# Kernel tuning notes

Measured on AMD Instinct MI355X. Metric: run time of the kernel, lower is better.

## Reference

```python
import jax, jax.numpy as jnp
import numpy as np

B, N, M = 4, 8192, 8192


def setup_inputs() -> dict:
    key = jax.random.key(0)
    k1, k2 = jax.random.split(key)
    xyz1 = jax.random.normal(k1, (B, N, 3), dtype=jnp.float32)
    xyz2 = jax.random.normal(k2, (B, M, 3), dtype=jnp.float32)
    return {"xyz1": xyz1, "xyz2": xyz2}


def reference(xyz1, xyz2):
    # Note: torch.cdist(p=2) returns sqrt(sq); min over sqrt == min over sq
    # (monotone), and the module squares afterward, so min of squared
    # distances is exactly equivalent (and avoids sqrt-at-0 grad issues).
    sq1 = jnp.sum(xyz1 * xyz1, axis=-1)  # (B, N)
    sq2 = jnp.sum(xyz2 * xyz2, axis=-1)  # (B, M)
    cross = jnp.einsum("bnd,bmd->bnm", xyz1, xyz2)  # (B, N, M)
    d2 = jnp.maximum(sq1[:, :, None] + sq2[:, None, :] - 2.0 * cross, 0.0)
    dist1 = jnp.min(d2, axis=2)  # (B, N) nearest in xyz2 for each xyz1 point
    dist2 = jnp.min(d2, axis=1)  # (B, M) nearest in xyz1 for each xyz2 point
    return jnp.mean(dist1) + jnp.mean(dist2)
```

## Files before the change

kernel.cpp:

```cpp
#include <hip/hip_runtime.h>
#include <math.h>

typedef short  bf16x8 __attribute__((ext_vector_type(8)));
typedef float  f32x16 __attribute__((ext_vector_type(16)));

constexpr int BATCH = 4, NPTS = 8192;
constexpr int CLOUD = BATCH * NPTS;

__device__ inline unsigned short bf16_rne(float x) {
    unsigned int u = __float_as_uint(x);
    return (unsigned short)((u + 0x7FFFu + ((u >> 16) & 1u)) >> 16);
}
__device__ inline float bf16_val(unsigned short h) {
    return __uint_as_float(((unsigned int)h) << 16);
}

__global__ __launch_bounds__(256) void cd_prep(
    const float* __restrict__ x1, const float* __restrict__ x2,
    uint4* __restrict__ APK, uint4* __restrict__ BPK,
    unsigned int* __restrict__ dist) {
    const int i = blockIdx.x * 256 + threadIdx.x;
    dist[i] = 0x7F800000u;
    const float* src = (i < CLOUD) ? x1 : x2;
    const int idx = i & (CLOUD - 1);
    const float x = src[idx*3+0], y = src[idx*3+1], z = src[idx*3+2];
    const float r = x*x + y*y + z*z;

    const unsigned short one = 0x3F80u;
    const unsigned short r0 = bf16_rne(r);
    const float rm1 = r - bf16_val(r0);
    const unsigned short r1 = bf16_rne(rm1);
    const unsigned short r2 = bf16_rne(rm1 - bf16_val(r1));

    const unsigned short hx = bf16_rne(x), hy = bf16_rne(y), hz = bf16_rne(z);
    const unsigned short lx = bf16_rne(x - bf16_val(hx));
    const unsigned short ly = bf16_rne(y - bf16_val(hy));
    const unsigned short lz = bf16_rne(z - bf16_val(hz));
    uint4 a0, a1;
    a0.x = (unsigned)hx | ((unsigned)lx << 16);
    a0.y = (unsigned)hx | ((unsigned)hy << 16);
    a0.z = (unsigned)ly | ((unsigned)hy << 16);
    a0.w = (unsigned)hz | ((unsigned)lz << 16);
    a1.x = (unsigned)hz | ((unsigned)one << 16);
    a1.y = (unsigned)one | ((unsigned)one << 16);
    a1.z = (unsigned)r0 | ((unsigned)r1 << 16);
    a1.w = (unsigned)r2;

    const float tx = -2.f*x, ty = -2.f*y, tz = -2.f*z;
    const unsigned short ax = bf16_rne(tx), ay = bf16_rne(ty), az = bf16_rne(tz);
    const unsigned short bx = bf16_rne(tx - bf16_val(ax));
    const unsigned short by = bf16_rne(ty - bf16_val(ay));
    const unsigned short bz = bf16_rne(tz - bf16_val(az));
    uint4 b0, b1;
    b0.x = (unsigned)ax | ((unsigned)ax << 16);
    b0.y = (unsigned)bx | ((unsigned)ay << 16);
    b0.z = (unsigned)ay | ((unsigned)by << 16);
    b0.w = (unsigned)az | ((unsigned)az << 16);
    b1.x = (unsigned)bz | ((unsigned)r0 << 16);
    b1.y = (unsigned)r1 | ((unsigned)r2 << 16);
    b1.z = (unsigned)one | ((unsigned)one << 16);
    b1.w = (unsigned)one;

    const int g = i >> 5, w = i & 31;
    APK[g*64 + w]      = a0;  APK[g*64 + 32 + w] = a1;
    BPK[g*64 + w]      = b0;  BPK[g*64 + 32 + w] = b1;
}

__global__ __launch_bounds__(256) void cd_gemm(
    const uint4* __restrict__ APK, const uint4* __restrict__ BPK,
    unsigned int* __restrict__ dist) {

    __shared__ uint4 Blds[2048];
    __shared__ float lbuf[4][32][33];

    const int tid = threadIdx.x;
    const int wv  = tid >> 6;
    const int l   = tid & 63;
    const int lane31 = l & 31, half = l >> 5;

    const int wid = blockIdx.x * 4 + wv;
    const int dir = wid >> 12;
    const int b   = (wid >> 10) & 3;
    const int cc  = (wid >> 7) & 7;
    const int rg  = wid & 127;

    const int aPt = (dir ? CLOUD : 0) + b * NPTS + rg * 64;
    const int bPt = (dir ? 0 : CLOUD) + b * NPTS + cc * 1024;

    {
        const uint4* src = BPK + (size_t)bPt * 2;
#pragma unroll
        for (int k = 0; k < 8; ++k)
            Blds[tid + k * 256] = src[tid + k * 256];
    }

    bf16x8 afr0, afr1;
    {
        uint4 v0 = APK[(size_t)aPt * 2 + l];
        uint4 v1 = APK[(size_t)aPt * 2 + 64 + l];
        __builtin_memcpy(&afr0, &v0, 16);
        __builtin_memcpy(&afr1, &v1, 16);
    }

    f32x16 zc;
#pragma unroll
    for (int i = 0; i < 16; ++i) zc[i] = 0.0f;

    float racc[2][16];
#pragma unroll
    for (int f = 0; f < 2; ++f)
#pragma unroll
        for (int r = 0; r < 16; ++r) racc[f][r] = INFINITY;

    __syncthreads();

#pragma unroll 4
    for (int p = 0; p < 16; ++p) {
        bf16x8 ba, bb;
        uint4 ua = Blds[(2*p + 0) * 64 + l];
        uint4 ub = Blds[(2*p + 1) * 64 + l];
        __builtin_memcpy(&ba, &ua, 16);
        __builtin_memcpy(&bb, &ub, 16);
        f32x16 c0 = __builtin_amdgcn_mfma_f32_32x32x16_bf16(afr0, ba, zc, 0, 0, 0);
        f32x16 c1 = __builtin_amdgcn_mfma_f32_32x32x16_bf16(afr0, bb, zc, 0, 0, 0);
        f32x16 c2 = __builtin_amdgcn_mfma_f32_32x32x16_bf16(afr1, ba, zc, 0, 0, 0);
        f32x16 c3 = __builtin_amdgcn_mfma_f32_32x32x16_bf16(afr1, bb, zc, 0, 0, 0);
#pragma unroll
        for (int r = 0; r < 16; ++r) {
            racc[0][r] = fminf(fminf(c0[r], c1[r]), racc[0][r]);
            racc[1][r] = fminf(fminf(c2[r], c3[r]), racc[1][r]);
        }
    }

    const int distBase = dir * CLOUD + b * NPTS + rg * 64;
#pragma unroll
    for (int f = 0; f < 2; ++f) {
#pragma unroll
        for (int r = 0; r < 16; ++r) {
            const int rl = (r & 3) + 8 * (r >> 2) + 4 * half;
            lbuf[wv][rl][lane31] = racc[f][r];
        }
        const int row = l >> 1;
        float m = INFINITY;
#pragma unroll
        for (int i = 0; i < 16; ++i)
            m = fminf(m, lbuf[wv][row][(l & 1) * 16 + i]);
        m = fminf(m, __shfl_xor(m, 1, 64));
        if ((l & 1) == 0)
            atomicMin(&dist[distBase + f * 32 + row],
                      __float_as_uint(fmaxf(m, 0.0f)));
    }
}

__global__ __launch_bounds__(1024) void cd_reduce(
    const float* __restrict__ dm , float* __restrict__ out) {
    __shared__ float sw[16];
    const int t = threadIdx.x;
    const float4* v = reinterpret_cast<const float4*>(dm);
    float s = 0.0f;
#pragma unroll 4
    for (int i = t; i < 2 * CLOUD / 4; i += 1024) {
        float4 x = v[i];
        s += (x.x + x.y) + (x.z + x.w);
    }
#pragma unroll
    for (int off = 32; off > 0; off >>= 1) s += __shfl_down(s, off, 64);
    if ((t & 63) == 0) sw[t >> 6] = s;
    __syncthreads();
    if (t == 0) {
        float tot = 0.0f;
#pragma unroll
        for (int w = 0; w < 16; ++w) tot += sw[w];
        out[0] = tot / (float)CLOUD;
    }
}

extern "C" void kernel_launch(void* const* d_in, const int* in_sizes, int n_in,
                              void* d_out, int out_size, void* d_ws, size_t ws_size,
                              hipStream_t stream) {
    const float* xyz1 = (const float*)d_in[0];
    const float* xyz2 = (const float*)d_in[1];
    unsigned int* dist = (unsigned int*)d_ws;
    uint4* APK = (uint4*)((char*)d_ws + 2u * CLOUD * 4u);
    uint4* BPK = (uint4*)((char*)d_ws + 2u * CLOUD * 4u + 2u * CLOUD * 32u);
    float* out = (float*)d_out;

    cd_prep<<<2 * CLOUD / 256, 256, 0, stream>>>(xyz1, xyz2, APK, BPK, dist);
    cd_gemm<<<2048, 256, 0, stream>>>(APK, BPK, dist);
    cd_reduce<<<1, 1024, 0, stream>>>((const float*)dist, out);
}
```

Measured before the change: 39.25 us.

## Fuse bf16 packing into GEMM kernel and replace atomics with partial-min reduction

The separate prep kernel is removed. Each block now reads raw xyz floats and packs its own B tile into LDS and its A fragments into registers, and the LDS tile is reused as the reduction scratch buffer. Per-row atomicMin on a global dist array is replaced by plain stores of per-column-chunk partial minima. A multi-block reduce kernel then takes the min over the 8 chunks and sums the results with a fixed-point 64-bit atomic and a last-block finalize. This saves a kernel launch and the packed-buffer round trip through memory, at the cost of redundant packing work in every block (each B tile is repacked by the blocks that share it) and a larger partial buffer.

```diff
diff --git a/kernel.cpp b/kernel.cpp
--- a/kernel.cpp
+++ b/kernel.cpp
@@ -7,76 +7,67 @@
 constexpr int BATCH = 4, NPTS = 8192;
 constexpr int CLOUD = BATCH * NPTS;
 
-__device__ inline unsigned short bf16_rne(float x) {
-    unsigned int u = __float_as_uint(x);
-    return (unsigned short)((u + 0x7FFFu + ((u >> 16) & 1u)) >> 16);
-}
-__device__ inline float bf16_val(unsigned short h) {
-    return __uint_as_float(((unsigned int)h) << 16);
-}
-
-__global__ __launch_bounds__(256) void cd_prep(
+__device__ inline unsigned bf16_rne(float x) {
+    unsigned u = __float_as_uint(x);
+    return (u + 0x7FFFu + ((u >> 16) & 1u)) >> 16;
+}
+__device__ inline float bf16_val(unsigned h) {
+    return __uint_as_float(h << 16);
+}
+
+struct Pack2 { uint4 s0, s1; };
+
+__device__ inline Pack2 packA(float x, float y, float z) {
+    const unsigned one = 0x3F80u;
+    const float r = x*x + y*y + z*z;
+    const unsigned r0 = bf16_rne(r);
+    const float rm1 = r - bf16_val(r0);
+    const unsigned r1 = bf16_rne(rm1);
+    const unsigned r2 = bf16_rne(rm1 - bf16_val(r1));
+    const unsigned hx = bf16_rne(x), hy = bf16_rne(y), hz = bf16_rne(z);
+    const unsigned lx = bf16_rne(x - bf16_val(hx));
+    const unsigned ly = bf16_rne(y - bf16_val(hy));
+    const unsigned lz = bf16_rne(z - bf16_val(hz));
+    Pack2 P;
+    P.s0.x = hx | (lx << 16);  P.s0.y = hx | (hy << 16);
+    P.s0.z = ly | (hy << 16);  P.s0.w = hz | (lz << 16);
+    P.s1.x = hz | (one << 16); P.s1.y = one | (one << 16);
+    P.s1.z = r0 | (r1 << 16);  P.s1.w = r2;
+    return P;
+}
+__device__ inline Pack2 packB(float x, float y, float z) {
+    const unsigned one = 0x3F80u;
+    const float r = x*x + y*y + z*z;
+    const unsigned r0 = bf16_rne(r);
+    const float rm1 = r - bf16_val(r0);
+    const unsigned r1 = bf16_rne(rm1);
+    const unsigned r2 = bf16_rne(rm1 - bf16_val(r1));
+    const float tx = -2.f*x, ty = -2.f*y, tz = -2.f*z;
+    const unsigned ax = bf16_rne(tx), ay = bf16_rne(ty), az = bf16_rne(tz);
+    const unsigned bx = bf16_rne(tx - bf16_val(ax));
+    const unsigned by = bf16_rne(ty - bf16_val(ay));
+    const unsigned bz = bf16_rne(tz - bf16_val(az));
+    Pack2 P;
+    P.s0.x = ax | (ax << 16);  P.s0.y = bx | (ay << 16);
+    P.s0.z = ay | (by << 16);  P.s0.w = az | (az << 16);
+    P.s1.x = bz | (r0 << 16);  P.s1.y = r1 | (r2 << 16);
+    P.s1.z = one | (one << 16);P.s1.w = one;
+    return P;
+}
+
+__global__ __launch_bounds__(256) void cd_main(
     const float* __restrict__ x1, const float* __restrict__ x2,
-    uint4* __restrict__ APK, uint4* __restrict__ BPK,
-    unsigned int* __restrict__ dist) {
-    const int i = blockIdx.x * 256 + threadIdx.x;
-    dist[i] = 0x7F800000u;
-    const float* src = (i < CLOUD) ? x1 : x2;
-    const int idx = i & (CLOUD - 1);
-    const float x = src[idx*3+0], y = src[idx*3+1], z = src[idx*3+2];
-    const float r = x*x + y*y + z*z;
-
-    const unsigned short one = 0x3F80u;
-    const unsigned short r0 = bf16_rne(r);
-    const float rm1 = r - bf16_val(r0);
-    const unsigned short r1 = bf16_rne(rm1);
-    const unsigned short r2 = bf16_rne(rm1 - bf16_val(r1));
-
-    const unsigned short hx = bf16_rne(x), hy = bf16_rne(y), hz = bf16_rne(z);
-    const unsigned short lx = bf16_rne(x - bf16_val(hx));
-    const unsigned short ly = bf16_rne(y - bf16_val(hy));
-    const unsigned short lz = bf16_rne(z - bf16_val(hz));
-    uint4 a0, a1;
-    a0.x = (unsigned)hx | ((unsigned)lx << 16);
-    a0.y = (unsigned)hx | ((unsigned)hy << 16);
-    a0.z = (unsigned)ly | ((unsigned)hy << 16);
-    a0.w = (unsigned)hz | ((unsigned)lz << 16);
-    a1.x = (unsigned)hz | ((unsigned)one << 16);
-    a1.y = (unsigned)one | ((unsigned)one << 16);
-    a1.z = (unsigned)r0 | ((unsigned)r1 << 16);
-    a1.w = (unsigned)r2;
-
-    const float tx = -2.f*x, ty = -2.f*y, tz = -2.f*z;
-    const unsigned short ax = bf16_rne(tx), ay = bf16_rne(ty), az = bf16_rne(tz);
-    const unsigned short bx = bf16_rne(tx - bf16_val(ax));
-    const unsigned short by = bf16_rne(ty - bf16_val(ay));
-    const unsigned short bz = bf16_rne(tz - bf16_val(az));
-    uint4 b0, b1;
-    b0.x = (unsigned)ax | ((unsigned)ax << 16);
-    b0.y = (unsigned)bx | ((unsigned)ay << 16);
-    b0.z = (unsigned)ay | ((unsigned)by << 16);
-    b0.w = (unsigned)az | ((unsigned)az << 16);
-    b1.x = (unsigned)bz | ((unsigned)r0 << 16);
-    b1.y = (unsigned)r1 | ((unsigned)r2 << 16);
-    b1.z = (unsigned)one | ((unsigned)one << 16);
-    b1.w = (unsigned)one;
-
-    const int g = i >> 5, w = i & 31;
-    APK[g*64 + w]      = a0;  APK[g*64 + 32 + w] = a1;
-    BPK[g*64 + w]      = b0;  BPK[g*64 + 32 + w] = b1;
-}
-
-__global__ __launch_bounds__(256) void cd_gemm(
-    const uint4* __restrict__ APK, const uint4* __restrict__ BPK,
-    unsigned int* __restrict__ dist) {
+    float* __restrict__ partial,
+    unsigned long long* __restrict__ total, unsigned int* __restrict__ counter) {
 
     __shared__ uint4 Blds[2048];
-    __shared__ float lbuf[4][32][33];
 
     const int tid = threadIdx.x;
     const int wv  = tid >> 6;
     const int l   = tid & 63;
     const int lane31 = l & 31, half = l >> 5;
+
+    if (blockIdx.x == 0 && tid == 0) { *total = 0ULL; *counter = 0u; }
 
     const int wid = blockIdx.x * 4 + wv;
     const int dir = wid >> 12;
@@ -84,22 +75,34 @@
     const int cc  = (wid >> 7) & 7;
     const int rg  = wid & 127;
 
-    const int aPt = (dir ? CLOUD : 0) + b * NPTS + rg * 64;
-    const int bPt = (dir ? 0 : CLOUD) + b * NPTS + cc * 1024;
-
     {
-        const uint4* src = BPK + (size_t)bPt * 2;
-#pragma unroll
-        for (int k = 0; k < 8; ++k)
-            Blds[tid + k * 256] = src[tid + k * 256];
+        const float* oth = dir ? x1 : x2;
+        const int othBase = b * NPTS + cc * 1024;
+        const float4* src =
+            reinterpret_cast<const float4*>(oth + (size_t)othBase * 3) + tid * 3;
+        float4 A = src[0], Q = src[1], C = src[2];
+        const float px[4] = {A.x, A.w, Q.z, C.y};
+        const float py[4] = {A.y, Q.x, Q.w, C.z};
+        const float pz[4] = {A.z, Q.y, C.x, C.w};
+#pragma unroll
+        for (int j = 0; j < 4; ++j) {
+            Pack2 P = packB(px[j], py[j], pz[j]);
+            const int pt = 4 * tid + j, g = pt >> 5, w = pt & 31;
+            Blds[g * 64 + w]      = P.s0;
+            Blds[g * 64 + 32 + w] = P.s1;
+        }
     }
 
     bf16x8 afr0, afr1;
     {
-        uint4 v0 = APK[(size_t)aPt * 2 + l];
-        uint4 v1 = APK[(size_t)aPt * 2 + 64 + l];
-        __builtin_memcpy(&afr0, &v0, 16);
-        __builtin_memcpy(&afr1, &v1, 16);
+        const float* own = dir ? x2 : x1;
+        const int r0i = (b * NPTS + rg * 64 + lane31) * 3;
+        Pack2 PA = packA(own[r0i], own[r0i + 1], own[r0i + 2]);
+        Pack2 PB = packA(own[r0i + 96], own[r0i + 97], own[r0i + 98]);
+        uint4 s0 = half ? PA.s1 : PA.s0;
+        uint4 s1 = half ? PB.s1 : PB.s0;
+        __builtin_memcpy(&afr0, &s0, 16);
+        __builtin_memcpy(&afr1, &s1, 16);
     }
 
     f32x16 zc;
@@ -123,55 +126,67 @@
         __builtin_memcpy(&bb, &ub, 16);
         f32x16 c0 = __builtin_amdgcn_mfma_f32_32x32x16_bf16(afr0, ba, zc, 0, 0, 0);
         f32x16 c1 = __builtin_amdgcn_mfma_f32_32x32x16_bf16(afr0, bb, zc, 0, 0, 0);
+#pragma unroll
+        for (int r = 0; r < 16; ++r)
+            racc[0][r] = fminf(fminf(c0[r], c1[r]), racc[0][r]);
         f32x16 c2 = __builtin_amdgcn_mfma_f32_32x32x16_bf16(afr1, ba, zc, 0, 0, 0);
         f32x16 c3 = __builtin_amdgcn_mfma_f32_32x32x16_bf16(afr1, bb, zc, 0, 0, 0);
 #pragma unroll
-        for (int r = 0; r < 16; ++r) {
-            racc[0][r] = fminf(fminf(c0[r], c1[r]), racc[0][r]);
+        for (int r = 0; r < 16; ++r)
             racc[1][r] = fminf(fminf(c2[r], c3[r]), racc[1][r]);
-        }
-    }
-
-    const int distBase = dir * CLOUD + b * NPTS + rg * 64;
+    }
+
+    __syncthreads();
+
+    float* lbuf = reinterpret_cast<float*>(Blds) + wv * (32 * 33);
+    const int pBase = (dir * 8 + cc) * CLOUD + b * NPTS + rg * 64;
 #pragma unroll
     for (int f = 0; f < 2; ++f) {
 #pragma unroll
         for (int r = 0; r < 16; ++r) {
             const int rl = (r & 3) + 8 * (r >> 2) + 4 * half;
-            lbuf[wv][rl][lane31] = racc[f][r];
+            lbuf[rl * 33 + lane31] = racc[f][r];
         }
         const int row = l >> 1;
         float m = INFINITY;
 #pragma unroll
         for (int i = 0; i < 16; ++i)
-            m = fminf(m, lbuf[wv][row][(l & 1) * 16 + i]);
+            m = fminf(m, lbuf[row * 33 + (l & 1) * 16 + i]);
         m = fminf(m, __shfl_xor(m, 1, 64));
         if ((l & 1) == 0)
-            atomicMin(&dist[distBase + f * 32 + row],
-                      __float_as_uint(fmaxf(m, 0.0f)));
-    }
-}
-
-__global__ __launch_bounds__(1024) void cd_reduce(
-    const float* __restrict__ dm , float* __restrict__ out) {
-    __shared__ float sw[16];
-    const int t = threadIdx.x;
-    const float4* v = reinterpret_cast<const float4*>(dm);
-    float s = 0.0f;
-#pragma unroll 4
-    for (int i = t; i < 2 * CLOUD / 4; i += 1024) {
-        float4 x = v[i];
-        s += (x.x + x.y) + (x.z + x.w);
+            partial[pBase + f * 32 + row] = fmaxf(m, 0.0f);
+    }
+}
+
+__global__ __launch_bounds__(256) void cd_reduce(
+    const float* __restrict__ partial,
+    unsigned long long* __restrict__ total, unsigned int* __restrict__ counter,
+    float* __restrict__ out) {
+    const int tid = threadIdx.x, bid = blockIdx.x;
+    double s = 0.0;
+#pragma unroll
+    for (int k = 0; k < 8; ++k) {
+        const int R  = bid * 2048 + k * 256 + tid;
+        const int d  = R >> 15, rr = R & 32767;
+        const float* pp = partial + (size_t)(d * 8) * CLOUD + rr;
+        float m = pp[0];
+#pragma unroll
+        for (int c = 1; c < 8; ++c) m = fminf(m, pp[(size_t)c * CLOUD]);
+        s += (double)m;
     }
 #pragma unroll
     for (int off = 32; off > 0; off >>= 1) s += __shfl_down(s, off, 64);
-    if ((t & 63) == 0) sw[t >> 6] = s;
-    __syncthreads();
-    if (t == 0) {
-        float tot = 0.0f;
-#pragma unroll
-        for (int w = 0; w < 16; ++w) tot += sw[w];
-        out[0] = tot / (float)CLOUD;
+    if ((tid & 63) == 0) {
+        const unsigned long long q =
+            (unsigned long long)(s * 1073741824.0 + 0.5);
+        atomicAdd(total, q);
+        __threadfence();
+        const unsigned old = atomicAdd(counter, 1u);
+        if (old == 127u) {
+            __threadfence();
+            const unsigned long long t = atomicAdd(total, 0ULL);
+            out[0] = (float)((double)t * (1.0 / 1073741824.0) / (double)CLOUD);
+        }
     }
 }
 
@@ -180,12 +195,12 @@
                               hipStream_t stream) {
     const float* xyz1 = (const float*)d_in[0];
     const float* xyz2 = (const float*)d_in[1];
-    unsigned int* dist = (unsigned int*)d_ws;
-    uint4* APK = (uint4*)((char*)d_ws + 2u * CLOUD * 4u);
-    uint4* BPK = (uint4*)((char*)d_ws + 2u * CLOUD * 4u + 2u * CLOUD * 32u);
+    float* partial = (float*)d_ws;
+    unsigned long long* total =
+        (unsigned long long*)((char*)d_ws + 16u * CLOUD * 4u);
+    unsigned int* counter = (unsigned int*)(total + 1);
     float* out = (float*)d_out;
 
-    cd_prep<<<2 * CLOUD / 256, 256, 0, stream>>>(xyz1, xyz2, APK, BPK, dist);
-    cd_gemm<<<2048, 256, 0, stream>>>(APK, BPK, dist);
-    cd_reduce<<<1, 1024, 0, stream>>>((const float*)dist, out);
-}
+    cd_main<<<2048, 256, 0, stream>>>(xyz1, xyz2, partial, total, counter);
+    cd_reduce<<<32, 256, 0, stream>>>(partial, total, counter, out);
+}
```

Result: no change. 39.49 us (+0.6%).
